# Optimization experiments

Hardware: AMD Instinct MI355X
Metric: run time of the kernel (lower is better)

Reference implementation:

```python
import jax, jax.numpy as jnp
import numpy as np

B, T, H, L = 8, 256, 64, 3
NB, NF, HP = 17, 68, 6
K = 9  # temporal kernel
PAD = (K - 1) // 2
EPS = 1e-5


def _normalize(adj):
    adj = adj + np.eye(adj.shape[0], dtype=np.float32)
    d = adj.sum(1)
    dinv = np.power(d, -0.5)
    dinv[np.isinf(dinv)] = 0.0
    return (dinv[:, None] * adj * dinv[None, :]).astype(np.float32)


def _body_adj():
    a = np.zeros((NB, NB), np.float32)
    conns = [(0, 1), (0, 2), (1, 3), (2, 4), (0, 5), (0, 6), (5, 6), (5, 7), (7, 9), (6, 8), (8, 10), (5, 11), (6, 12), (11, 12), (11, 13), (13, 15), (12, 14), (14, 16)]
    for i, j in conns:
        a[i, j] = 1.0
        a[j, i] = 1.0
    return _normalize(a)


def _face_adj():
    a = np.zeros((NF, NF), np.float32)
    for i in range(16): a[i, i + 1] = 1.0
    for i in range(17, 21): a[i, i + 1] = 1.0
    for i in range(22, 26): a[i, i + 1] = 1.0
    for i in range(27, 30): a[i, i + 1] = 1.0
    for i in range(31, 35): a[i, i + 1] = 1.0
    for i in range(36, 41): a[i, i + 1] = 1.0
    a[41, 36] = 1.0
    for i in range(42, 47): a[i, i + 1] = 1.0
    a[47, 42] = 1.0
    for i in range(48, 59): a[i, i + 1] = 1.0
    a[59, 48] = 1.0
    for i in range(60, 67): a[i, i + 1] = 1.0
    a[67, 60] = 1.0
    a = a + a.T
    return _normalize(a)


def setup_inputs() -> dict:
    keys = iter(jax.random.split(jax.random.key(0), 80))

    def rn(shape, s):
        return jax.random.normal(next(keys), shape, jnp.float32) * s

    inp = {}
    inp['body_kps'] = jax.random.normal(next(keys), (B, T, NB * 2), jnp.float32)
    inp['face_kps_2d'] = jax.random.normal(next(keys), (B, T, NF * 2), jnp.float32)
    inp['head_pose'] = jax.random.normal(next(keys), (B, T, HP), jnp.float32)
    inp['body_adj'] = jnp.asarray(_body_adj())
    inp['face_adj'] = jnp.asarray(_face_adj())
    inp['body_proj_w'] = rn((2, H), 0.5)
    inp['body_proj_b'] = jnp.zeros((H,), jnp.float32)
    inp['face_proj_w'] = rn((2, H), 0.5)
    inp['face_proj_b'] = jnp.zeros((H,), jnp.float32)
    inp['head_w'] = rn((HP, H), 0.3)
    inp['head_b'] = jnp.zeros((H,), jnp.float32)
    for p in ('b', 'f'):
        inp[p + '_t1w'] = rn((L, H, H, K), 0.04)
        inp[p + '_t1b'] = jnp.zeros((L, H), jnp.float32)
        inp[p + '_bn1g'] = jnp.ones((L, H), jnp.float32)
        inp[p + '_bn1b'] = jnp.zeros((L, H), jnp.float32)
        inp[p + '_bn1m'] = rn((L, H), 0.1)
        inp[p + '_bn1v'] = jax.random.uniform(next(keys), (L, H), jnp.float32, 0.5, 1.5)
        inp[p + '_gcw'] = rn((L, H, H), 0.1)
        inp[p + '_gcb'] = jnp.zeros((L, H), jnp.float32)
        inp[p + '_t2w'] = rn((L, H, H, K), 0.04)
        inp[p + '_t2b'] = jnp.zeros((L, H), jnp.float32)
        inp[p + '_bn2g'] = jnp.ones((L, H), jnp.float32)
        inp[p + '_bn2b'] = jnp.zeros((L, H), jnp.float32)
        inp[p + '_bn2m'] = rn((L, H), 0.1)
        inp[p + '_bn2v'] = jax.random.uniform(next(keys), (L, H), jnp.float32, 0.5, 1.5)
    total = NB * H + NF * H + H  # 5504
    inp['fus1_w'] = rn((total, 4 * H), 0.02)
    inp['fus1_b'] = jnp.zeros((4 * H,), jnp.float32)
    inp['fus2_w'] = rn((4 * H, 2 * H), 0.06)
    inp['fus2_b'] = jnp.zeros((2 * H,), jnp.float32)
    inp['fus3_w'] = rn((2 * H, H), 0.09)
    inp['fus3_b'] = jnp.zeros((H,), jnp.float32)
    inp['fus4_w'] = rn((H, 5), 0.12)
    inp['fus4_b'] = jnp.zeros((5,), jnp.float32)
    return inp


def _conv_bn(x, w, b, g, be, m, v):
    # x: (BN, C, T); w: (O, I, K). Conv1d (pad=4) + eval-mode BatchNorm1d.
    y = jax.lax.conv_general_dilated(x, w, (1,), [(PAD, PAD)], dimension_numbers=('NCH', 'OIH', 'NCH'))
    y = y + b[None, :, None]
    inv = g * jax.lax.rsqrt(v + EPS)
    return y * inv[None, :, None] + (be - m * inv)[None, :, None]


def _block(x, adj, t1w, t1b, g1, b1, m1, v1, gw, gb, t2w, t2b, g2, b2, m2, v2):
    # x: (B, N, C, T); residual is identity (in_channels == out_channels)
    Bn, N, C, Tn = x.shape
    res = x
    h = jax.nn.relu(_conv_bn(x.reshape(Bn * N, C, Tn), t1w, t1b, g1, b1, m1, v1)).reshape(Bn, N, C, Tn)
    # spatial graph conv, batched over all timesteps at once (adj @ (x W) + b)
    support = jnp.einsum('bnct,co->bnot', h, gw)
    h = jax.nn.relu(jnp.einsum('mn,bnot->bmot', adj, support) + gb[None, None, :, None])
    h = _conv_bn(h.reshape(Bn * N, C, Tn), t2w, t2b, g2, b2, m2, v2).reshape(Bn, N, C, Tn)
    return h + res  # dropout = identity in eval


def _stream(x, n_nodes, pw, pb, adj, ps):
    Bn, Tn, _ = x.shape
    h = x.reshape(Bn, Tn, n_nodes, 2) @ pw + pb          # (B, T, N, H)
    h = jnp.transpose(h, (0, 2, 3, 1))                   # (B, N, H, T)
    for l in range(ps[0].shape[0]):
        h = _block(h, adj, *(p[l] for p in ps))
    return h.mean(axis=3).reshape(Bn, -1)                # temporal mean-pool, flatten nodes


def reference(body_kps, face_kps_2d, head_pose, body_adj, face_adj, body_proj_w, body_proj_b, face_proj_w, face_proj_b, head_w, head_b, b_t1w, b_t1b, b_bn1g, b_bn1b, b_bn1m, b_bn1v, b_gcw, b_gcb, b_t2w, b_t2b, b_bn2g, b_bn2b, b_bn2m, b_bn2v, f_t1w, f_t1b, f_bn1g, f_bn1b, f_bn1m, f_bn1v, f_gcw, f_gcb, f_t2w, f_t2b, f_bn2g, f_bn2b, f_bn2m, f_bn2v, fus1_w, fus1_b, fus2_w, fus2_b, fus3_w, fus3_b, fus4_w, fus4_b):
    bps = (b_t1w, b_t1b, b_bn1g, b_bn1b, b_bn1m, b_bn1v, b_gcw, b_gcb, b_t2w, b_t2b, b_bn2g, b_bn2b, b_bn2m, b_bn2v)
    fps = (f_t1w, f_t1b, f_bn1g, f_bn1b, f_bn1m, f_bn1v, f_gcw, f_gcb, f_t2w, f_t2b, f_bn2g, f_bn2b, f_bn2m, f_bn2v)
    bf = _stream(body_kps, NB, body_proj_w, body_proj_b, body_adj, bps)
    ff = _stream(face_kps_2d, NF, face_proj_w, face_proj_b, face_adj, fps)
    hp = jax.nn.relu(head_pose @ head_w + head_b).mean(axis=1)
    feat = jnp.concatenate([bf, ff, hp], axis=-1)
    h = jax.nn.relu(feat @ fus1_w + fus1_b)
    h = jax.nn.relu(h @ fus2_w + fus2_b)
    h = jax.nn.relu(h @ fus3_w + fus3_b)
    return h @ fus4_w + fus4_b
```

## Files before the change

kernel.cpp:

```cpp
#include <hip/hip_runtime.h>

constexpr int B_ = 8, T_ = 256, H_ = 64, L_ = 3, NB_ = 17, NF_ = 68, HP_ = 6, K_ = 9;
constexpr int FEAT_DIM = NB_ * H_ + NF_ * H_ + H_;
constexpr int HT = H_ * T_;

typedef _Float16 half4_t __attribute__((ext_vector_type(4)));
typedef _Float16 half8_t __attribute__((ext_vector_type(8)));
typedef float f32x16 __attribute__((ext_vector_type(16)));
typedef float f32x4 __attribute__((ext_vector_type(4)));

constexpr size_t SZ_AB = (size_t)B_ * NB_ * HT;
constexpr size_t SZ_AF = (size_t)B_ * NF_ * HT;
constexpr size_t OFF_TB   = 0;
constexpr size_t OFF_TF   = OFF_TB + SZ_AB / 2;
constexpr size_t OFF_SUPB = OFF_TF + SZ_AF / 2;
constexpr size_t OFF_SUPF = OFF_SUPB + SZ_AB / 2;
constexpr size_t OFF_GB   = OFF_SUPF + SZ_AF / 2;
constexpr size_t OFF_GF   = OFF_GB + SZ_AB / 2;
constexpr size_t OFF_W3   = OFF_GF + SZ_AF / 2;
constexpr size_t OFF_GW3  = OFF_W3 + 4 * 55296;
constexpr size_t OFF_B2   = OFF_GW3 + 2 * 6144;
constexpr size_t OFF_ADJPB= OFF_B2 + 768;
constexpr size_t OFF_ADJPF= OFF_ADJPB + 512;
constexpr size_t OFF_FEAT = OFF_ADJPF + 3840;
constexpr size_t OFF_P1   = OFF_FEAT + (size_t)B_ * FEAT_DIM;

struct ConvPrepSet { const float *w, *tb, *g, *bb, *m, *v; };

__global__ __launch_bounds__(256) void prep_convW_all(ConvPrepSet s0, ConvPrepSet s1,
                                                      ConvPrepSet s2, ConvPrepSet s3,
                                                      _Float16* __restrict__ w3,
                                                      float* __restrict__ b2) {
    int set = blockIdx.y;
    ConvPrepSet s = (set == 0) ? s0 : (set == 1) ? s1 : (set == 2) ? s2 : s3;
    int idx = blockIdx.x * 256 + threadIdx.x;
    int k = idx % K_; int r = idx / K_;
    int i = r % H_; r /= H_;
    int o = r % H_; int l = r / H_;
    float sc = s.g[l * H_ + o] * rsqrtf(s.v[l * H_ + o] + 1e-5f);
    w3[(size_t)set * 110592 + ((((l * K_ + k) * 8 + (i >> 3)) * H_ + o) * 8) + (i & 7)]
        = (_Float16)(s.w[idx] * sc);
    if (i == 0 && k == 0)
        b2[set * 192 + l * H_ + o] =
            s.tb[l * H_ + o] * sc + s.bb[l * H_ + o] - s.m[l * H_ + o] * sc;
}

__global__ __launch_bounds__(256) void prep_gcw_all(const float* __restrict__ g0,
                                                    const float* __restrict__ g1,
                                                    _Float16* __restrict__ w3) {
    int set = blockIdx.y;
    const float* gw = set ? g1 : g0;
    int idx = blockIdx.x * 256 + threadIdx.x;
    int o = idx % H_; int r = idx / H_;
    int c = r % H_; int l = r / H_;
    w3[(size_t)set * 12288 + (((l * 8 + (c >> 3)) * H_ + o) * 8) + (c & 7)] = (_Float16)gw[idx];
}

__global__ __launch_bounds__(256) void prep_misc(const float* __restrict__ adjB,
                                                 const float* __restrict__ adjF,
                                                 _Float16* __restrict__ pB,
                                                 _Float16* __restrict__ pF,
                                                 float* __restrict__ p1,
                                                 float* __restrict__ feat) {
    int idx = blockIdx.x * 256 + threadIdx.x;
    if (idx < 1024) {
        int m = idx >> 5, k = idx & 31;
        pB[idx] = (m < NB_ && k < NB_) ? (_Float16)adjB[m * NB_ + k] : (_Float16)0.f;
    } else if (idx < 8704) {
        int j = idx - 1024;
        int m = j / 80, k = j % 80;
        pF[j] = (m < NF_ && k < NF_) ? (_Float16)adjF[m * NF_ + k] : (_Float16)0.f;
    } else if (idx < 10752) {
        p1[idx - 8704] = 0.f;
    } else if (idx < 10752 + B_ * FEAT_DIM) {
        feat[idx - 10752] = 0.f;
    }
}

__global__ __launch_bounds__(256) void proj_kernel(const float* __restrict__ kpsB,
                                                   const float* __restrict__ pwB,
                                                   const float* __restrict__ pbB,
                                                   _Float16* __restrict__ outB,
                                                   const float* __restrict__ kpsF,
                                                   const float* __restrict__ pwF,
                                                   const float* __restrict__ pbF,
                                                   _Float16* __restrict__ outF,
                                                   const float* __restrict__ hx,
                                                   const float* __restrict__ hw,
                                                   const float* __restrict__ hb,
                                                   float* __restrict__ feat,
                                                   int nblk0, int nblk1) {
    int blk = blockIdx.x;
    if (blk >= nblk1) {
        int b = blk - nblk1;
        int c = threadIdx.x;
        if (c >= 64) return;
        float w0 = hw[c], w1 = hw[64 + c], w2 = hw[128 + c],
              w3 = hw[192 + c], w4 = hw[256 + c], w5 = hw[320 + c];
        float bias = hb[c];
        float acc = 0.f;
        for (int t = 0; t < T_; ++t) {
            const float* xr = hx + ((size_t)b * T_ + t) * HP_;
            float s = fmaf(xr[0], w0, fmaf(xr[1], w1, fmaf(xr[2], w2,
                      fmaf(xr[3], w3, fmaf(xr[4], w4, fmaf(xr[5], w5, bias))))));
            acc += fmaxf(s, 0.f);
        }
        feat[(size_t)b * FEAT_DIM + NB_ * H_ + NF_ * H_ + c] = acc * (1.f / 256.f);
        return;
    }
    const float *kps, *pw, *pb; _Float16* out; int N, bn;
    if (blk < nblk0) { kps = kpsB; pw = pwB; pb = pbB; out = outB; N = NB_; bn = blk; }
    else { kps = kpsF; pw = pwF; pb = pbF; out = outF; N = NF_; bn = blk - nblk0; }
    int b = bn / N, n = bn % N;
    int t = threadIdx.x;
    float x0 = kps[((size_t)b * T_ + t) * (N * 2) + n * 2 + 0];
    float x1 = kps[((size_t)b * T_ + t) * (N * 2) + n * 2 + 1];
    _Float16* ob = out + (size_t)bn * HT + t;
#pragma unroll 8
    for (int c = 0; c < H_; ++c)
        ob[(size_t)c * T_] = (_Float16)fmaf(x0, pw[c], fmaf(x1, pw[H_ + c], pb[c]));
}

__device__ __forceinline__ half8_t ld_b8(const _Float16* p) {
    half4_t lo = *(const half4_t*)p;
    half4_t hi = *(const half4_t*)(p + 4);
    return __builtin_shufflevector(lo, hi, 0, 1, 2, 3, 4, 5, 6, 7);
}

__device__ __forceinline__ void stage_full(const _Float16* __restrict__ xb,
                                           _Float16* __restrict__ Xs, int tid) {
    for (int u = tid; u < 8 * 264; u += 256) {
        int oct = u / 264;
        int row = u - oct * 264;
        int t = row - 4;
        _Float16 v[8];
        if (t >= 0 && t < T_) {
            const _Float16* xr = xb + (size_t)(oct * 8) * T_ + t;
#pragma unroll
            for (int j = 0; j < 8; ++j) v[j] = xr[(size_t)j * T_];
        } else {
#pragma unroll
            for (int j = 0; j < 8; ++j) v[j] = (_Float16)0.f;
        }
        _Float16* dst = &Xs[row * 68 + oct * 8];
        half4_t lo, hi;
#pragma unroll
        for (int j = 0; j < 4; ++j) { lo[j] = v[j]; hi[j] = v[4 + j]; }
        *(half4_t*)dst = lo;
        *(half4_t*)(dst + 4) = hi;
    }
}

struct CM {
    const _Float16* x; const half8_t* w1; const float* b1; const half8_t* gc; _Float16* sup;
};

__global__ __launch_bounds__(256, 2) void convmix_kernel(CM P0, CM P1, int nblk0, int l) {
    __shared__ __align__(16) _Float16 Xs[264 * 68];
    int blk = blockIdx.x;
    CM P = (blk < nblk0) ? P0 : P1;
    if (blk >= nblk0) blk -= nblk0;
    int bn = blk;
    int tid = threadIdx.x;
    stage_full(P.x + (size_t)bn * HT, Xs, tid);
    __syncthreads();

    int ln = tid & 63;
    int w = __builtin_amdgcn_readfirstlane(tid >> 6);
    int ln31 = ln & 31, kg = ln >> 5;
    int tw = w * 64;

    f32x16 acc[2][2];
#pragma unroll
    for (int mt = 0; mt < 2; ++mt)
#pragma unroll
        for (int f = 0; f < 2; ++f)
#pragma unroll
            for (int r = 0; r < 16; ++r) acc[mt][f][r] = 0.f;

    const half8_t* wl = P.w1 + (size_t)l * (K_ * 8 * H_);
    const _Float16* xr0 = Xs + (size_t)(tw + ln31) * 68;
#pragma unroll
    for (int tap = 0; tap < K_; ++tap) {
#pragma unroll
        for (int ks = 0; ks < 4; ++ks) {
            int i8 = ks * 2 + kg;
            half8_t a0 = wl[(tap * 8 + i8) * H_ + ln31];
            half8_t a1 = wl[(tap * 8 + i8) * H_ + 32 + ln31];
            half8_t b0 = ld_b8(xr0 + tap * 68 + i8 * 8);
            half8_t b1 = ld_b8(xr0 + (32 + tap) * 68 + i8 * 8);
            acc[0][0] = __builtin_amdgcn_mfma_f32_32x32x16_f16(a0, b0, acc[0][0], 0, 0, 0);
            acc[0][1] = __builtin_amdgcn_mfma_f32_32x32x16_f16(a0, b1, acc[0][1], 0, 0, 0);
            acc[1][0] = __builtin_amdgcn_mfma_f32_32x32x16_f16(a1, b0, acc[1][0], 0, 0, 0);
            acc[1][1] = __builtin_amdgcn_mfma_f32_32x32x16_f16(a1, b1, acc[1][1], 0, 0, 0);
        }
    }
    __syncthreads();

    {
#pragma unroll
        for (int f = 0; f < 2; ++f) {
            _Float16* mrow = Xs + (size_t)(4 + tw + f * 32 + ln31) * 68;
#pragma unroll
            for (int mt = 0; mt < 2; ++mt) {
#pragma unroll
                for (int rg = 0; rg < 4; ++rg) {
                    int o0 = mt * 32 + rg * 8 + kg * 4;
                    f32x4 bv = *(const f32x4*)(P.b1 + l * H_ + o0);
                    half4_t hv;
#pragma unroll
                    for (int j = 0; j < 4; ++j)
                        hv[j] = (_Float16)fmaxf(acc[mt][f][rg * 4 + j] + bv[j], 0.f);
                    *(half4_t*)(mrow + o0) = hv;
                }
            }
        }
    }
    __syncthreads();

    f32x16 acc2[2][2];
#pragma unroll
    for (int mt = 0; mt < 2; ++mt)
#pragma unroll
        for (int f = 0; f < 2; ++f)
#pragma unroll
            for (int r = 0; r < 16; ++r) acc2[mt][f][r] = 0.f;
    const half8_t* gl = P.gc + (size_t)l * (8 * H_);
    const _Float16* mrow0 = Xs + (size_t)(4 + tw + ln31) * 68;
#pragma unroll
    for (int ks = 0; ks < 4; ++ks) {
        int i8 = ks * 2 + kg;
        half8_t a0 = gl[i8 * H_ + ln31];
        half8_t a1 = gl[i8 * H_ + 32 + ln31];
        half8_t b0 = ld_b8(mrow0 + i8 * 8);
        half8_t b1 = ld_b8(mrow0 + 32 * 68 + i8 * 8);
        acc2[0][0] = __builtin_amdgcn_mfma_f32_32x32x16_f16(a0, b0, acc2[0][0], 0, 0, 0);
        acc2[0][1] = __builtin_amdgcn_mfma_f32_32x32x16_f16(a0, b1, acc2[0][1], 0, 0, 0);
        acc2[1][0] = __builtin_amdgcn_mfma_f32_32x32x16_f16(a1, b0, acc2[1][0], 0, 0, 0);
        acc2[1][1] = __builtin_amdgcn_mfma_f32_32x32x16_f16(a1, b1, acc2[1][1], 0, 0, 0);
    }

    _Float16* sp = P.sup + (size_t)bn * HT;
#pragma unroll
    for (int mt = 0; mt < 2; ++mt) {
#pragma unroll
        for (int f = 0; f < 2; ++f) {
            int t = tw + f * 32 + ln31;
#pragma unroll
            for (int r = 0; r < 16; ++r) {
                int o = mt * 32 + (r & 3) + 8 * (r >> 2) + 4 * kg;
                sp[(size_t)o * T_ + t] = (_Float16)acc2[mt][f][r];
            }
        }
    }
}

struct C2 {
    const _Float16* x; const half8_t* w2; const float* b2; _Float16* trunk; int N; int fbase;
};

template <bool LAST>
__global__ __launch_bounds__(256, 2) void conv2_kernel(C2 P0, C2 P1, int nblk0, int l,
                                                       float* __restrict__ feat) {
    __shared__ __align__(16) _Float16 Xs[264 * 68];
    int blk = blockIdx.x;
    C2 P = (blk < nblk0) ? P0 : P1;
    if (blk >= nblk0) blk -= nblk0;
    int bn = blk;
    int tid = threadIdx.x;
    stage_full(P.x + (size_t)bn * HT, Xs, tid);
    __syncthreads();

    int ln = tid & 63;
    int w = __builtin_amdgcn_readfirstlane(tid >> 6);
    int ln31 = ln & 31, kg = ln >> 5;
    int tw = w * 64;

    f32x16 acc[2][2];
#pragma unroll
    for (int mt = 0; mt < 2; ++mt)
#pragma unroll
        for (int f = 0; f < 2; ++f)
#pragma unroll
            for (int r = 0; r < 16; ++r) acc[mt][f][r] = 0.f;

    const half8_t* wl = P.w2 + (size_t)l * (K_ * 8 * H_);
    const _Float16* xr0 = Xs + (size_t)(tw + ln31) * 68;
#pragma unroll
    for (int tap = 0; tap < K_; ++tap) {
#pragma unroll
        for (int ks = 0; ks < 4; ++ks) {
            int i8 = ks * 2 + kg;
            half8_t a0 = wl[(tap * 8 + i8) * H_ + ln31];
            half8_t a1 = wl[(tap * 8 + i8) * H_ + 32 + ln31];
            half8_t b0 = ld_b8(xr0 + tap * 68 + i8 * 8);
            half8_t b1 = ld_b8(xr0 + (32 + tap) * 68 + i8 * 8);
            acc[0][0] = __builtin_amdgcn_mfma_f32_32x32x16_f16(a0, b0, acc[0][0], 0, 0, 0);
            acc[0][1] = __builtin_amdgcn_mfma_f32_32x32x16_f16(a0, b1, acc[0][1], 0, 0, 0);
            acc[1][0] = __builtin_amdgcn_mfma_f32_32x32x16_f16(a1, b0, acc[1][0], 0, 0, 0);
            acc[1][1] = __builtin_amdgcn_mfma_f32_32x32x16_f16(a1, b1, acc[1][1], 0, 0, 0);
        }
    }

    const _Float16* resb = P.trunk + (size_t)bn * HT;
    if (!LAST) {
        _Float16* tob = P.trunk + (size_t)bn * HT;
#pragma unroll
        for (int mt = 0; mt < 2; ++mt) {
#pragma unroll
            for (int f = 0; f < 2; ++f) {
                int t = tw + f * 32 + ln31;
#pragma unroll
                for (int r = 0; r < 16; ++r) {
                    int o = mt * 32 + (r & 3) + 8 * (r >> 2) + 4 * kg;
                    float y = acc[mt][f][r] + P.b2[l * H_ + o] + (float)resb[(size_t)o * T_ + t];
                    tob[(size_t)o * T_ + t] = (_Float16)y;
                }
            }
        }
    } else {
        __syncthreads();
        float* red = (float*)Xs;
        float sv[2][16];
#pragma unroll
        for (int mt = 0; mt < 2; ++mt) {
#pragma unroll
            for (int r = 0; r < 16; ++r) {
                int o = mt * 32 + (r & 3) + 8 * (r >> 2) + 4 * kg;
                float b2v = P.b2[l * H_ + o];
                float s = (acc[mt][0][r] + b2v + (float)resb[(size_t)o * T_ + tw + ln31])
                        + (acc[mt][1][r] + b2v + (float)resb[(size_t)o * T_ + tw + 32 + ln31]);
#pragma unroll
                for (int off = 1; off < 32; off <<= 1) s += __shfl_xor(s, off);
                sv[mt][r] = s;
            }
        }
        if (ln31 == 0) {
#pragma unroll
            for (int mt = 0; mt < 2; ++mt)
#pragma unroll
                for (int r = 0; r < 16; ++r) {
                    int o = mt * 32 + (r & 3) + 8 * (r >> 2) + 4 * kg;
                    red[w * 64 + o] = sv[mt][r];
                }
        }
        __syncthreads();
        if (tid < 64) {
            float s = red[tid] + red[64 + tid] + red[128 + tid] + red[192 + tid];
            int b = bn / P.N, n = bn % P.N;
            atomicAdd(&feat[(size_t)b * FEAT_DIM + P.fbase + n * H_ + tid], s * (1.f / 256.f));
        }
    }
}

template <int N, int MT, int KS>
__device__ __forceinline__ void adjmix_impl(const _Float16* __restrict__ sup,
                                            const half8_t* __restrict__ adjP,
                                            const float* __restrict__ gb,
                                            _Float16* __restrict__ out,
                                            int blk, int l, _Float16* Ls, int tid) {
    constexpr int KP = KS * 16;
    constexpr int PITCH = KP + 4;
    int b = blk >> 7, cb = blk & 127;
    int colbase = cb * 128;
    float gbv = gb[l * H_ + (cb >> 1)];

    for (int u = tid; u < KP * 16; u += 256) {
        int n = u >> 4, cs = u & 15;
        half8_t v;
        if (n < N) v = *(const half8_t*)(sup + (size_t)(b * N + n) * HT + colbase + cs * 8);
        else {
#pragma unroll
            for (int j = 0; j < 8; ++j) v[j] = (_Float16)0.f;
        }
#pragma unroll
        for (int j = 0; j < 8; ++j) Ls[(cs * 8 + j) * PITCH + n] = v[j];
    }
    __syncthreads();

    int ln = tid & 63;
    int w = __builtin_amdgcn_readfirstlane(tid >> 6);
    int ln31 = ln & 31, kg = ln >> 5;
    int colL = w * 32 + ln31;

    f32x16 acc[MT];
#pragma unroll
    for (int mt = 0; mt < MT; ++mt)
#pragma unroll
        for (int r = 0; r < 16; ++r) acc[mt][r] = 0.f;

#pragma unroll
    for (int ks = 0; ks < KS; ++ks) {
        half8_t bf = ld_b8(&Ls[colL * PITCH + ks * 16 + kg * 8]);
#pragma unroll
        for (int mt = 0; mt < MT; ++mt) {
            half8_t af = adjP[(size_t)(mt * 32 + ln31) * (KP / 8) + ks * 2 + kg];
            acc[mt] = __builtin_amdgcn_mfma_f32_32x32x16_f16(af, bf, acc[mt], 0, 0, 0);
        }
    }

    int col = colbase + colL;
#pragma unroll
    for (int mt = 0; mt < MT; ++mt) {
#pragma unroll
        for (int r = 0; r < 16; ++r) {
            int m = mt * 32 + (r & 3) + 8 * (r >> 2) + 4 * kg;
            if (m < N)
                out[(size_t)(b * N + m) * HT + col] = (_Float16)fmaxf(acc[mt][r] + gbv, 0.f);
        }
    }
}

__global__ __launch_bounds__(256) void adjmix_kernel(
        const _Float16* __restrict__ supB, const half8_t* __restrict__ adjPB,
        const float* __restrict__ gbB, _Float16* __restrict__ outB,
        const _Float16* __restrict__ supF, const half8_t* __restrict__ adjPF,
        const float* __restrict__ gbF, _Float16* __restrict__ outF,
        int nblk0, int l) {
    __shared__ __align__(16) _Float16 Ls[128 * 84];
    int blk = blockIdx.x, tid = threadIdx.x;
    if (blk < nblk0)
        adjmix_impl<NB_, 1, 2>(supB, adjPB, gbB, outB, blk, l, Ls, tid);
    else
        adjmix_impl<NF_, 3, 5>(supF, adjPF, gbF, outF, blk - nblk0, l, Ls, tid);
}

__global__ __launch_bounds__(256) void fus1_kernel(const float* __restrict__ feat,
                                                   const float* __restrict__ w1,
                                                   float* __restrict__ p1) {
    __shared__ float fv[128];
    int b = blockIdx.x / 43, ic = blockIdx.x % 43;
    int tid = threadIdx.x;
    if (tid < 128) fv[tid] = feat[(size_t)b * FEAT_DIM + ic * 128 + tid];
    __syncthreads();
    const float* wb = w1 + (size_t)(ic * 128) * 256 + tid;
    float acc = 0.f;
#pragma unroll 4
    for (int i = 0; i < 128; ++i)
        acc = fmaf(fv[i], wb[(size_t)i * 256], acc);
    atomicAdd(&p1[b * 256 + tid], acc);
}

__global__ __launch_bounds__(256) void fus_tail_kernel(const float* __restrict__ p1,
        const float* __restrict__ b1, const float* __restrict__ w2, const float* __restrict__ b2,
        const float* __restrict__ w3, const float* __restrict__ b3,
        const float* __restrict__ w4, const float* __restrict__ b4, float* __restrict__ out) {
    __shared__ float s1[256], s2[128], s3[64];
    int b = blockIdx.x, tid = threadIdx.x;
    s1[tid] = fmaxf(p1[b * 256 + tid] + b1[tid], 0.f);
    __syncthreads();
    if (tid < 128) {
        float acc = b2[tid];
        for (int i = 0; i < 256; ++i) acc = fmaf(s1[i], w2[i * 128 + tid], acc);
        s2[tid] = fmaxf(acc, 0.f);
    }
    __syncthreads();
    if (tid < 64) {
        float acc = b3[tid];
        for (int i = 0; i < 128; ++i) acc = fmaf(s2[i], w3[i * 64 + tid], acc);
        s3[tid] = fmaxf(acc, 0.f);
    }
    __syncthreads();
    if (tid < 5) {
        float acc = b4[tid];
        for (int i = 0; i < 64; ++i) acc = fmaf(s3[i], w4[i * 5 + tid], acc);
        out[b * 5 + tid] = acc;
    }
}

extern "C" void kernel_launch(void* const* d_in, const int* in_sizes, int n_in,
                              void* d_out, int out_size, void* d_ws, size_t ws_size,
                              hipStream_t stream) {
    const float* body_kps = (const float*)d_in[0];
    const float* face_kps = (const float*)d_in[1];
    const float* head_pose = (const float*)d_in[2];
    const float* body_adj = (const float*)d_in[3];
    const float* face_adj = (const float*)d_in[4];
    const float* body_pw = (const float*)d_in[5];
    const float* body_pb = (const float*)d_in[6];
    const float* face_pw = (const float*)d_in[7];
    const float* face_pb = (const float*)d_in[8];
    const float* head_w = (const float*)d_in[9];
    const float* head_b = (const float*)d_in[10];
    const float* b_t1w = (const float*)d_in[11]; const float* b_t1b = (const float*)d_in[12];
    const float* b_g1  = (const float*)d_in[13]; const float* b_b1  = (const float*)d_in[14];
    const float* b_m1  = (const float*)d_in[15]; const float* b_v1  = (const float*)d_in[16];
    const float* b_gcw = (const float*)d_in[17]; const float* b_gcb = (const float*)d_in[18];
    const float* b_t2w = (const float*)d_in[19]; const float* b_t2b = (const float*)d_in[20];
    const float* b_g2  = (const float*)d_in[21]; const float* b_b2  = (const float*)d_in[22];
    const float* b_m2  = (const float*)d_in[23]; const float* b_v2  = (const float*)d_in[24];
    const float* f_t1w = (const float*)d_in[25]; const float* f_t1b = (const float*)d_in[26];
    const float* f_g1  = (const float*)d_in[27]; const float* f_b1  = (const float*)d_in[28];
    const float* f_m1  = (const float*)d_in[29]; const float* f_v1  = (const float*)d_in[30];
    const float* f_gcw = (const float*)d_in[31]; const float* f_gcb = (const float*)d_in[32];
    const float* f_t2w = (const float*)d_in[33]; const float* f_t2b = (const float*)d_in[34];
    const float* f_g2  = (const float*)d_in[35]; const float* f_b2  = (const float*)d_in[36];
    const float* f_m2  = (const float*)d_in[37]; const float* f_v2  = (const float*)d_in[38];
    const float* fus1_w = (const float*)d_in[39]; const float* fus1_b = (const float*)d_in[40];
    const float* fus2_w = (const float*)d_in[41]; const float* fus2_b = (const float*)d_in[42];
    const float* fus3_w = (const float*)d_in[43]; const float* fus3_b = (const float*)d_in[44];
    const float* fus4_w = (const float*)d_in[45]; const float* fus4_b = (const float*)d_in[46];

    float* ws = (float*)d_ws;
    _Float16* TrB = (_Float16*)(ws + OFF_TB);
    _Float16* TrF = (_Float16*)(ws + OFF_TF);
    _Float16* SupB = (_Float16*)(ws + OFF_SUPB);
    _Float16* SupF = (_Float16*)(ws + OFF_SUPF);
    _Float16* Gb = (_Float16*)(ws + OFF_GB);
    _Float16* Gf = (_Float16*)(ws + OFF_GF);
    _Float16* W3 = (_Float16*)(ws + OFF_W3);
    _Float16* W3b1 = W3;            _Float16* W3b2 = W3 + 110592;
    _Float16* W3f1 = W3 + 221184;   _Float16* W3f2 = W3 + 331776;
    _Float16* GW3 = (_Float16*)(ws + OFF_GW3);
    _Float16* GW3b = GW3;           _Float16* GW3f = GW3 + 12288;
    float* B2 = ws + OFF_B2;
    float* B2b1 = B2;        float* B2b2 = B2 + 192;
    float* B2f1 = B2 + 384;  float* B2f2 = B2 + 576;
    _Float16* adjPB = (_Float16*)(ws + OFF_ADJPB);
    _Float16* adjPF = (_Float16*)(ws + OFF_ADJPF);
    float* feat = ws + OFF_FEAT;
    float* p1 = ws + OFF_P1;
    float* out = (float*)d_out;

    ConvPrepSet sb1{b_t1w, b_t1b, b_g1, b_b1, b_m1, b_v1};
    ConvPrepSet sb2{b_t2w, b_t2b, b_g2, b_b2, b_m2, b_v2};
    ConvPrepSet sf1{f_t1w, f_t1b, f_g1, f_b1, f_m1, f_v1};
    ConvPrepSet sf2{f_t2w, f_t2b, f_g2, f_b2, f_m2, f_v2};
    prep_convW_all<<<dim3(432, 4), 256, 0, stream>>>(sb1, sb2, sf1, sf2, W3, B2);
    prep_gcw_all<<<dim3(48, 2), 256, 0, stream>>>(b_gcw, f_gcw, GW3);
    prep_misc<<<214, 256, 0, stream>>>(body_adj, face_adj, adjPB, adjPF, p1, feat);

    const int nB = B_ * NB_;
    const int nF = B_ * NF_;
    proj_kernel<<<nB + nF + B_, 256, 0, stream>>>(body_kps, body_pw, body_pb, TrB,
                                                  face_kps, face_pw, face_pb, TrF,
                                                  head_pose, head_w, head_b, feat,
                                                  nB, nB + nF);

    CM cmb{TrB, (const half8_t*)W3b1, B2b1, (const half8_t*)GW3b, SupB};
    CM cmf{TrF, (const half8_t*)W3f1, B2f1, (const half8_t*)GW3f, SupF};
    C2 c2b{Gb, (const half8_t*)W3b2, B2b2, TrB, NB_, 0};
    C2 c2f{Gf, (const half8_t*)W3f2, B2f2, TrF, NF_, NB_ * H_};

    const int gc = nB + nF;
    const int n0 = nB;
    const int ga = B_ * 128;

    for (int l = 0; l < L_; ++l) {
        convmix_kernel<<<gc, 256, 0, stream>>>(cmb, cmf, n0, l);
        adjmix_kernel<<<2 * ga, 256, 0, stream>>>(SupB, (const half8_t*)adjPB, b_gcb, Gb,
                                                  SupF, (const half8_t*)adjPF, f_gcb, Gf, ga, l);
        if (l < L_ - 1)
            conv2_kernel<false><<<gc, 256, 0, stream>>>(c2b, c2f, n0, l, feat);
        else
            conv2_kernel<true><<<gc, 256, 0, stream>>>(c2b, c2f, n0, l, feat);
    }

    fus1_kernel<<<B_ * 43, 256, 0, stream>>>(feat, fus1_w, p1);
    fus_tail_kernel<<<B_, 256, 0, stream>>>(p1, fus1_b, fus2_w, fus2_b, fus3_w, fus3_b,
                                            fus4_w, fus4_b, out);
}
```

Before: 394.0 us.

## Switch activations to time-major layout with LDS-staged vectorized stores, merge prep kernels

The intermediate activation layout changes from channel-major [node][channel][time] to time-major [node][time][channel]. This makes staging loads, residual reads and output writes in the conv, adjacency-mix and projection kernels contiguous 16-byte vector accesses instead of strided scalar ones, with outputs passed through shared memory first. Separately, the three prep kernels are merged into one launch, and fus1 is restructured so each weight load is reused across all 8 batches. The cost is extra LDS (a residual tile in conv2) and extra barriers, which may reduce occupancy.

```diff
diff --git a/kernel.cpp b/kernel.cpp
--- a/kernel.cpp
+++ b/kernel.cpp
@@ -27,53 +27,57 @@
 
 struct ConvPrepSet { const float *w, *tb, *g, *bb, *m, *v; };
 
-__global__ __launch_bounds__(256) void prep_convW_all(ConvPrepSet s0, ConvPrepSet s1,
-                                                      ConvPrepSet s2, ConvPrepSet s3,
-                                                      _Float16* __restrict__ w3,
-                                                      float* __restrict__ b2) {
-    int set = blockIdx.y;
-    ConvPrepSet s = (set == 0) ? s0 : (set == 1) ? s1 : (set == 2) ? s2 : s3;
-    int idx = blockIdx.x * 256 + threadIdx.x;
-    int k = idx % K_; int r = idx / K_;
-    int i = r % H_; r /= H_;
-    int o = r % H_; int l = r / H_;
-    float sc = s.g[l * H_ + o] * rsqrtf(s.v[l * H_ + o] + 1e-5f);
-    w3[(size_t)set * 110592 + ((((l * K_ + k) * 8 + (i >> 3)) * H_ + o) * 8) + (i & 7)]
-        = (_Float16)(s.w[idx] * sc);
-    if (i == 0 && k == 0)
-        b2[set * 192 + l * H_ + o] =
-            s.tb[l * H_ + o] * sc + s.bb[l * H_ + o] - s.m[l * H_ + o] * sc;
-}
-
-__global__ __launch_bounds__(256) void prep_gcw_all(const float* __restrict__ g0,
-                                                    const float* __restrict__ g1,
-                                                    _Float16* __restrict__ w3) {
-    int set = blockIdx.y;
-    const float* gw = set ? g1 : g0;
-    int idx = blockIdx.x * 256 + threadIdx.x;
-    int o = idx % H_; int r = idx / H_;
-    int c = r % H_; int l = r / H_;
-    w3[(size_t)set * 12288 + (((l * 8 + (c >> 3)) * H_ + o) * 8) + (c & 7)] = (_Float16)gw[idx];
-}
-
-__global__ __launch_bounds__(256) void prep_misc(const float* __restrict__ adjB,
-                                                 const float* __restrict__ adjF,
-                                                 _Float16* __restrict__ pB,
-                                                 _Float16* __restrict__ pF,
-                                                 float* __restrict__ p1,
-                                                 float* __restrict__ feat) {
-    int idx = blockIdx.x * 256 + threadIdx.x;
-    if (idx < 1024) {
-        int m = idx >> 5, k = idx & 31;
-        pB[idx] = (m < NB_ && k < NB_) ? (_Float16)adjB[m * NB_ + k] : (_Float16)0.f;
-    } else if (idx < 8704) {
-        int j = idx - 1024;
-        int m = j / 80, k = j % 80;
-        pF[j] = (m < NF_ && k < NF_) ? (_Float16)adjF[m * NF_ + k] : (_Float16)0.f;
-    } else if (idx < 10752) {
-        p1[idx - 8704] = 0.f;
-    } else if (idx < 10752 + B_ * FEAT_DIM) {
-        feat[idx - 10752] = 0.f;
+__global__ __launch_bounds__(256) void prep_all(ConvPrepSet s0, ConvPrepSet s1,
+                                                ConvPrepSet s2, ConvPrepSet s3,
+                                                _Float16* __restrict__ w3,
+                                                float* __restrict__ b2,
+                                                const float* __restrict__ g0,
+                                                const float* __restrict__ g1,
+                                                _Float16* __restrict__ gw3,
+                                                const float* __restrict__ adjB,
+                                                const float* __restrict__ adjF,
+                                                _Float16* __restrict__ pB,
+                                                _Float16* __restrict__ pF,
+                                                float* __restrict__ p1,
+                                                float* __restrict__ feat) {
+    int blk = blockIdx.x;
+    int tid = threadIdx.x;
+    if (blk < 1728) {
+        int set = blk / 432;
+        int bx = blk % 432;
+        ConvPrepSet s = (set == 0) ? s0 : (set == 1) ? s1 : (set == 2) ? s2 : s3;
+        int idx = bx * 256 + tid;
+        int k = idx % K_; int r = idx / K_;
+        int i = r % H_; r /= H_;
+        int o = r % H_; int l = r / H_;
+        float sc = s.g[l * H_ + o] * rsqrtf(s.v[l * H_ + o] + 1e-5f);
+        w3[(size_t)set * 110592 + ((((l * K_ + k) * 8 + (i >> 3)) * H_ + o) * 8) + (i & 7)]
+            = (_Float16)(s.w[idx] * sc);
+        if (i == 0 && k == 0)
+            b2[set * 192 + l * H_ + o] =
+                s.tb[l * H_ + o] * sc + s.bb[l * H_ + o] - s.m[l * H_ + o] * sc;
+    } else if (blk < 1824) {
+        int set = (blk - 1728) / 48;
+        int bx = (blk - 1728) % 48;
+        const float* gw = set ? g1 : g0;
+        int idx = bx * 256 + tid;
+        int o = idx % H_; int r = idx / H_;
+        int c = r % H_; int l = r / H_;
+        gw3[(size_t)set * 12288 + (((l * 8 + (c >> 3)) * H_ + o) * 8) + (c & 7)] = (_Float16)gw[idx];
+    } else {
+        int idx = (blk - 1824) * 256 + tid;
+        if (idx < 1024) {
+            int m = idx >> 5, k = idx & 31;
+            pB[idx] = (m < NB_ && k < NB_) ? (_Float16)adjB[m * NB_ + k] : (_Float16)0.f;
+        } else if (idx < 8704) {
+            int j = idx - 1024;
+            int m = j / 80, k = j % 80;
+            pF[j] = (m < NF_ && k < NF_) ? (_Float16)adjF[m * NF_ + k] : (_Float16)0.f;
+        } else if (idx < 10752) {
+            p1[idx - 8704] = 0.f;
+        } else if (idx < 10752 + B_ * FEAT_DIM) {
+            feat[idx - 10752] = 0.f;
+        }
     }
 }
 
@@ -115,10 +119,17 @@
     int t = threadIdx.x;
     float x0 = kps[((size_t)b * T_ + t) * (N * 2) + n * 2 + 0];
     float x1 = kps[((size_t)b * T_ + t) * (N * 2) + n * 2 + 1];
-    _Float16* ob = out + (size_t)bn * HT + t;
-#pragma unroll 8
-    for (int c = 0; c < H_; ++c)
-        ob[(size_t)c * T_] = (_Float16)fmaf(x0, pw[c], fmaf(x1, pw[H_ + c], pb[c]));
+    _Float16* ob = out + (size_t)bn * HT + (size_t)t * H_;
+#pragma unroll
+    for (int cg = 0; cg < 8; ++cg) {
+        half8_t v;
+#pragma unroll
+        for (int j = 0; j < 8; ++j) {
+            int c = cg * 8 + j;
+            v[j] = (_Float16)fmaf(x0, pw[c], fmaf(x1, pw[H_ + c], pb[c]));
+        }
+        *(half8_t*)(ob + cg * 8) = v;
+    }
 }
 
 __device__ __forceinline__ half8_t ld_b8(const _Float16* p) {
@@ -127,27 +138,36 @@
     return __builtin_shufflevector(lo, hi, 0, 1, 2, 3, 4, 5, 6, 7);
 }
 
+__device__ __forceinline__ void st_b8(_Float16* p, half8_t v) {
+    half4_t lo, hi;
+#pragma unroll
+    for (int j = 0; j < 4; ++j) { lo[j] = v[j]; hi[j] = v[4 + j]; }
+    *(half4_t*)p = lo;
+    *(half4_t*)(p + 4) = hi;
+}
+
 __device__ __forceinline__ void stage_full(const _Float16* __restrict__ xb,
                                            _Float16* __restrict__ Xs, int tid) {
-    for (int u = tid; u < 8 * 264; u += 256) {
-        int oct = u / 264;
-        int row = u - oct * 264;
+    for (int u = tid; u < 264 * 8; u += 256) {
+        int row = u >> 3, c = u & 7;
         int t = row - 4;
-        _Float16 v[8];
+        half8_t v;
         if (t >= 0 && t < T_) {
-            const _Float16* xr = xb + (size_t)(oct * 8) * T_ + t;
-#pragma unroll
-            for (int j = 0; j < 8; ++j) v[j] = xr[(size_t)j * T_];
+            v = *(const half8_t*)(xb + (size_t)t * H_ + c * 8);
         } else {
 #pragma unroll
             for (int j = 0; j < 8; ++j) v[j] = (_Float16)0.f;
         }
-        _Float16* dst = &Xs[row * 68 + oct * 8];
-        half4_t lo, hi;
-#pragma unroll
-        for (int j = 0; j < 4; ++j) { lo[j] = v[j]; hi[j] = v[4 + j]; }
-        *(half4_t*)dst = lo;
-        *(half4_t*)(dst + 4) = hi;
+        st_b8(&Xs[row * 68 + c * 8], v);
+    }
+}
+
+__device__ __forceinline__ void stage_res(const _Float16* __restrict__ xb,
+                                          _Float16* __restrict__ Rs, int tid) {
+    for (int u = tid; u < 256 * 8; u += 256) {
+        int row = u >> 3, c = u & 7;
+        half8_t v = *(const half8_t*)(xb + (size_t)row * H_ + c * 8);
+        st_b8(&Rs[row * 68 + c * 8], v);
     }
 }
 
@@ -197,22 +217,20 @@
     }
     __syncthreads();
 
-    {
-#pragma unroll
-        for (int f = 0; f < 2; ++f) {
-            _Float16* mrow = Xs + (size_t)(4 + tw + f * 32 + ln31) * 68;
-#pragma unroll
-            for (int mt = 0; mt < 2; ++mt) {
-#pragma unroll
-                for (int rg = 0; rg < 4; ++rg) {
-                    int o0 = mt * 32 + rg * 8 + kg * 4;
-                    f32x4 bv = *(const f32x4*)(P.b1 + l * H_ + o0);
-                    half4_t hv;
-#pragma unroll
-                    for (int j = 0; j < 4; ++j)
-                        hv[j] = (_Float16)fmaxf(acc[mt][f][rg * 4 + j] + bv[j], 0.f);
-                    *(half4_t*)(mrow + o0) = hv;
-                }
+#pragma unroll
+    for (int f = 0; f < 2; ++f) {
+        _Float16* mrow = Xs + (size_t)(4 + tw + f * 32 + ln31) * 68;
+#pragma unroll
+        for (int mt = 0; mt < 2; ++mt) {
+#pragma unroll
+            for (int rg = 0; rg < 4; ++rg) {
+                int o0 = mt * 32 + rg * 8 + kg * 4;
+                f32x4 bv = *(const f32x4*)(P.b1 + l * H_ + o0);
+                half4_t hv;
+#pragma unroll
+                for (int j = 0; j < 4; ++j)
+                    hv[j] = (_Float16)fmaxf(acc[mt][f][rg * 4 + j] + bv[j], 0.f);
+                *(half4_t*)(mrow + o0) = hv;
             }
         }
     }
@@ -240,18 +258,31 @@
         acc2[1][1] = __builtin_amdgcn_mfma_f32_32x32x16_f16(a1, b1, acc2[1][1], 0, 0, 0);
     }
 
-    _Float16* sp = P.sup + (size_t)bn * HT;
-#pragma unroll
-    for (int mt = 0; mt < 2; ++mt) {
-#pragma unroll
-        for (int f = 0; f < 2; ++f) {
-            int t = tw + f * 32 + ln31;
-#pragma unroll
-            for (int r = 0; r < 16; ++r) {
-                int o = mt * 32 + (r & 3) + 8 * (r >> 2) + 4 * kg;
-                sp[(size_t)o * T_ + t] = (_Float16)acc2[mt][f][r];
+#pragma unroll
+    for (int f = 0; f < 2; ++f) {
+        _Float16* orow = Xs + (size_t)(4 + tw + f * 32 + ln31) * 68;
+#pragma unroll
+        for (int mt = 0; mt < 2; ++mt) {
+#pragma unroll
+            for (int rg = 0; rg < 4; ++rg) {
+                int o0 = mt * 32 + rg * 8 + kg * 4;
+                half4_t hv;
+#pragma unroll
+                for (int j = 0; j < 4; ++j)
+                    hv[j] = (_Float16)acc2[mt][f][rg * 4 + j];
+                *(half4_t*)(orow + o0) = hv;
             }
         }
+    }
+    __syncthreads();
+    _Float16* gout = P.sup + (size_t)bn * HT + (size_t)tw * H_;
+    const _Float16* srow = Xs + (size_t)(4 + tw) * 68;
+#pragma unroll
+    for (int k2 = 0; k2 < 8; ++k2) {
+        int u = k2 * 64 + ln;
+        int r = u >> 3, c = u & 7;
+        half8_t v = ld_b8(srow + r * 68 + c * 8);
+        *(half8_t*)(gout + (size_t)r * H_ + c * 8) = v;
     }
 }
 
@@ -263,12 +294,14 @@
 __global__ __launch_bounds__(256, 2) void conv2_kernel(C2 P0, C2 P1, int nblk0, int l,
                                                        float* __restrict__ feat) {
     __shared__ __align__(16) _Float16 Xs[264 * 68];
+    __shared__ __align__(16) _Float16 Rs[256 * 68];
     int blk = blockIdx.x;
     C2 P = (blk < nblk0) ? P0 : P1;
     if (blk >= nblk0) blk -= nblk0;
     int bn = blk;
     int tid = threadIdx.x;
     stage_full(P.x + (size_t)bn * HT, Xs, tid);
+    stage_res(P.trunk + (size_t)bn * HT, Rs, tid);
     __syncthreads();
 
     int ln = tid & 63;
@@ -302,39 +335,61 @@
         }
     }
 
-    const _Float16* resb = P.trunk + (size_t)bn * HT;
     if (!LAST) {
-        _Float16* tob = P.trunk + (size_t)bn * HT;
-#pragma unroll
-        for (int mt = 0; mt < 2; ++mt) {
-#pragma unroll
-            for (int f = 0; f < 2; ++f) {
-                int t = tw + f * 32 + ln31;
-#pragma unroll
-                for (int r = 0; r < 16; ++r) {
-                    int o = mt * 32 + (r & 3) + 8 * (r >> 2) + 4 * kg;
-                    float y = acc[mt][f][r] + P.b2[l * H_ + o] + (float)resb[(size_t)o * T_ + t];
-                    tob[(size_t)o * T_ + t] = (_Float16)y;
+        __syncthreads();
+#pragma unroll
+        for (int f = 0; f < 2; ++f) {
+            int row = tw + f * 32 + ln31;
+            _Float16* orow = Xs + (size_t)(4 + row) * 68;
+            const _Float16* rrow = Rs + (size_t)row * 68;
+#pragma unroll
+            for (int mt = 0; mt < 2; ++mt) {
+#pragma unroll
+                for (int rg = 0; rg < 4; ++rg) {
+                    int o0 = mt * 32 + rg * 8 + kg * 4;
+                    f32x4 bv = *(const f32x4*)(P.b2 + l * H_ + o0);
+                    half4_t rv = *(const half4_t*)(rrow + o0);
+                    half4_t hv;
+#pragma unroll
+                    for (int j = 0; j < 4; ++j)
+                        hv[j] = (_Float16)(acc[mt][f][rg * 4 + j] + bv[j] + (float)rv[j]);
+                    *(half4_t*)(orow + o0) = hv;
                 }
             }
         }
+        __syncthreads();
+        _Float16* gout = P.trunk + (size_t)bn * HT + (size_t)tw * H_;
+        const _Float16* srow = Xs + (size_t)(4 + tw) * 68;
+#pragma unroll
+        for (int k2 = 0; k2 < 8; ++k2) {
+            int u = k2 * 64 + ln;
+            int r = u >> 3, c = u & 7;
+            half8_t v = ld_b8(srow + r * 68 + c * 8);
+            *(half8_t*)(gout + (size_t)r * H_ + c * 8) = v;
+        }
     } else {
+        float sv[2][16];
+#pragma unroll
+        for (int mt = 0; mt < 2; ++mt) {
+#pragma unroll
+            for (int rg = 0; rg < 4; ++rg) {
+                int o0 = mt * 32 + rg * 8 + kg * 4;
+                f32x4 bv = *(const f32x4*)(P.b2 + l * H_ + o0);
+                half4_t r0 = *(const half4_t*)(Rs + (size_t)(tw + ln31) * 68 + o0);
+                half4_t r1 = *(const half4_t*)(Rs + (size_t)(tw + 32 + ln31) * 68 + o0);
+#pragma unroll
+                for (int j = 0; j < 4; ++j) {
+                    int r = rg * 4 + j;
+                    float s = (acc[mt][0][r] + bv[j] + (float)r0[j])
+                            + (acc[mt][1][r] + bv[j] + (float)r1[j]);
+#pragma unroll
+                    for (int off = 1; off < 32; off <<= 1) s += __shfl_xor(s, off);
+                    sv[mt][r] = s;
+                }
+            }
+        }
         __syncthreads();
         float* red = (float*)Xs;
-        float sv[2][16];
-#pragma unroll
-        for (int mt = 0; mt < 2; ++mt) {
-#pragma unroll
-            for (int r = 0; r < 16; ++r) {
-                int o = mt * 32 + (r & 3) + 8 * (r >> 2) + 4 * kg;
-                float b2v = P.b2[l * H_ + o];
-                float s = (acc[mt][0][r] + b2v + (float)resb[(size_t)o * T_ + tw + ln31])
-                        + (acc[mt][1][r] + b2v + (float)resb[(size_t)o * T_ + tw + 32 + ln31]);
-#pragma unroll
-                for (int off = 1; off < 32; off <<= 1) s += __shfl_xor(s, off);
-                sv[mt][r] = s;
-            }
-        }
         if (ln31 == 0) {
 #pragma unroll
             for (int mt = 0; mt < 2; ++mt)
@@ -363,7 +418,6 @@
     constexpr int PITCH = KP + 4;
     int b = blk >> 7, cb = blk & 127;
     int colbase = cb * 128;
-    float gbv = gb[l * H_ + (cb >> 1)];
 
     for (int u = tid; u < KP * 16; u += 256) {
         int n = u >> 4, cs = u & 15;
@@ -398,16 +452,23 @@
             acc[mt] = __builtin_amdgcn_mfma_f32_32x32x16_f16(af, bf, acc[mt], 0, 0, 0);
         }
     }
-
-    int col = colbase + colL;
+    __syncthreads();
+
+    float gbv = gb[l * H_ + (colL & 63)];
 #pragma unroll
     for (int mt = 0; mt < MT; ++mt) {
 #pragma unroll
         for (int r = 0; r < 16; ++r) {
             int m = mt * 32 + (r & 3) + 8 * (r >> 2) + 4 * kg;
-            if (m < N)
-                out[(size_t)(b * N + m) * HT + col] = (_Float16)fmaxf(acc[mt][r] + gbv, 0.f);
-        }
+            Ls[m * 132 + colL] = (_Float16)fmaxf(acc[mt][r] + gbv, 0.f);
+        }
+    }
+    __syncthreads();
+
+    for (int u = tid; u < N * 16; u += 256) {
+        int m = u >> 4, c = u & 15;
+        half8_t v = ld_b8(&Ls[m * 132 + c * 8]);
+        *(half8_t*)(out + (size_t)(b * N + m) * HT + colbase + c * 8) = v;
     }
 }
 
@@ -417,7 +478,7 @@
         const _Float16* __restrict__ supF, const half8_t* __restrict__ adjPF,
         const float* __restrict__ gbF, _Float16* __restrict__ outF,
         int nblk0, int l) {
-    __shared__ __align__(16) _Float16 Ls[128 * 84];
+    __shared__ __align__(16) _Float16 Ls[12800];
     int blk = blockIdx.x, tid = threadIdx.x;
     if (blk < nblk0)
         adjmix_impl<NB_, 1, 2>(supB, adjPB, gbB, outB, blk, l, Ls, tid);
@@ -428,17 +489,27 @@
 __global__ __launch_bounds__(256) void fus1_kernel(const float* __restrict__ feat,
                                                    const float* __restrict__ w1,
                                                    float* __restrict__ p1) {
-    __shared__ float fv[128];
-    int b = blockIdx.x / 43, ic = blockIdx.x % 43;
+    __shared__ float fv[8][64];
+    int blk = blockIdx.x;
+    int ic = blk >> 1, kh = blk & 1;
+    int base = ic * 128 + kh * 64;
     int tid = threadIdx.x;
-    if (tid < 128) fv[tid] = feat[(size_t)b * FEAT_DIM + ic * 128 + tid];
-    __syncthreads();
-    const float* wb = w1 + (size_t)(ic * 128) * 256 + tid;
-    float acc = 0.f;
-#pragma unroll 4
-    for (int i = 0; i < 128; ++i)
-        acc = fmaf(fv[i], wb[(size_t)i * 256], acc);
-    atomicAdd(&p1[b * 256 + tid], acc);
+    for (int u = tid; u < 8 * 64; u += 256) {
+        int b = u >> 6, j = u & 63;
+        fv[b][j] = feat[(size_t)b * FEAT_DIM + base + j];
+    }
+    __syncthreads();
+    float acc[8];
+#pragma unroll
+    for (int b = 0; b < 8; ++b) acc[b] = 0.f;
+    const float* wb = w1 + (size_t)base * 256 + tid;
+    for (int i = 0; i < 64; ++i) {
+        float wv = wb[(size_t)i * 256];
+#pragma unroll
+        for (int b = 0; b < 8; ++b) acc[b] = fmaf(fv[b][i], wv, acc[b]);
+    }
+#pragma unroll
+    for (int b = 0; b < 8; ++b) atomicAdd(&p1[b * 256 + tid], acc[b]);
 }
 
 __global__ __launch_bounds__(256) void fus_tail_kernel(const float* __restrict__ p1,
@@ -526,9 +597,9 @@
     ConvPrepSet sb2{b_t2w, b_t2b, b_g2, b_b2, b_m2, b_v2};
     ConvPrepSet sf1{f_t1w, f_t1b, f_g1, f_b1, f_m1, f_v1};
     ConvPrepSet sf2{f_t2w, f_t2b, f_g2, f_b2, f_m2, f_v2};
-    prep_convW_all<<<dim3(432, 4), 256, 0, stream>>>(sb1, sb2, sf1, sf2, W3, B2);
-    prep_gcw_all<<<dim3(48, 2), 256, 0, stream>>>(b_gcw, f_gcw, GW3);
-    prep_misc<<<214, 256, 0, stream>>>(body_adj, face_adj, adjPB, adjPF, p1, feat);
+    prep_all<<<2038, 256, 0, stream>>>(sb1, sb2, sf1, sf2, W3, B2,
+                                       b_gcw, f_gcw, GW3,
+                                       body_adj, face_adj, adjPB, adjPF, p1, feat);
 
     const int nB = B_ * NB_;
     const int nF = B_ * NF_;
@@ -556,7 +627,7 @@
             conv2_kernel<true><<<gc, 256, 0, stream>>>(c2b, c2f, n0, l, feat);
     }
 
-    fus1_kernel<<<B_ * 43, 256, 0, stream>>>(feat, fus1_w, p1);
+    fus1_kernel<<<86, 256, 0, stream>>>(feat, fus1_w, p1);
     fus_tail_kernel<<<B_, 256, 0, stream>>>(p1, fus1_b, fus2_w, fus2_b, fus3_w, fus3_b,
                                             fus4_w, fus4_b, out);
 }
```

Measured after the change: 383.2 us. 1.03x faster.
